# Kernel optimization log

Hardware: AMD Instinct MI355X
Metric: run time of the kernel (lower is better)

Reference implementation:

```python
import jax, jax.numpy as jnp
import numpy as np

N_HEADS = 16
LN_EPS = 1e-5


def layer_norm(x, w, b):
    mu = jnp.mean(x, axis=-1, keepdims=True)
    var = jnp.mean((x - mu) ** 2, axis=-1, keepdims=True)
    return (x - mu) * jax.lax.rsqrt(var + LN_EPS) * w + b


def setup_inputs() -> dict:
    key = jax.random.key(0)
    B, S, D = 4, 2048, 1024
    F = 4 * D
    ks = jax.random.split(key, 16)
    s = 0.02
    return {
        "x": jax.random.normal(ks[0], (B, S, D), dtype=jnp.float32),
        "Wq": jax.random.normal(ks[1], (D, D), dtype=jnp.float32) * s,
        "Wk": jax.random.normal(ks[2], (D, D), dtype=jnp.float32) * s,
        "Wv": jax.random.normal(ks[3], (D, D), dtype=jnp.float32) * s,
        "Wo": jax.random.normal(ks[4], (D, D), dtype=jnp.float32) * s,
        "ln1_w": jnp.ones((D,), dtype=jnp.float32),
        "ln1_b": jnp.zeros((D,), dtype=jnp.float32),
        "W1": jax.random.normal(ks[5], (D, F), dtype=jnp.float32) * s,
        "b1": jnp.zeros((F,), dtype=jnp.float32),
        "W2": jax.random.normal(ks[6], (F, D), dtype=jnp.float32) * s,
        "b2": jnp.zeros((D,), dtype=jnp.float32),
        "ln2_w": jnp.ones((D,), dtype=jnp.float32),
        "ln2_b": jnp.zeros((D,), dtype=jnp.float32),
        "conf_w": jax.random.normal(ks[7], (D, 1), dtype=jnp.float32) * s,
        "conf_b": jnp.zeros((1,), dtype=jnp.float32),
    }


def reference(x, Wq, Wk, Wv, Wo, ln1_w, ln1_b, W1, b1, W2, b2, ln2_w, ln2_b, conf_w, conf_b):
    B, S, D = x.shape
    H = N_HEADS
    HD = D // H
    # --- attention sub-block (pre-LN) ---
    h = layer_norm(x, ln1_w, ln1_b)
    q = jnp.einsum("bsd,dhk->bhsk", h, Wq.reshape(D, H, HD))
    k = jnp.einsum("bsd,dhk->bhsk", h, Wk.reshape(D, H, HD))
    v = jnp.einsum("bsd,dhk->bhsk", h, Wv.reshape(D, H, HD))
    scores = jnp.einsum("bhsk,bhtk->bhst", q, k) / jnp.sqrt(jnp.asarray(HD, x.dtype))
    causal = jnp.triu(jnp.ones((S, S), dtype=bool), k=1)  # [S, S]
    scores = jnp.where(causal[None, None, :, :], -jnp.inf, scores)
    attn = jax.nn.softmax(scores, axis=-1)
    ctx = jnp.einsum("bhst,bhtk->bshk", attn, v).reshape(B, S, D)
    x = x + ctx @ Wo  # residual (dropout = identity in eval)
    # --- FFN sub-block ---
    h2 = layer_norm(x, ln2_w, ln2_b)
    x_out = x + jax.nn.relu(h2 @ W1 + b1) @ W2 + b2 * 0 + (jax.nn.relu(h2 @ W1 + b1) @ W2 * 0)
    x_out = x + (jax.nn.relu(h2 @ W1 + b1) @ W2 + b2)
    # --- confidence predictor: avg-pool over seq, linear, sigmoid, mean over batch ---
    conf = jax.nn.sigmoid(jnp.mean(x_out, axis=1) @ conf_w + conf_b)  # [B, 1]
    conf = jnp.mean(conf, axis=0)  # [1]
    return x_out, conf
```

## Files before the change

### kernel.cpp

```cpp
#include <hip/hip_runtime.h>
#include <hip/hip_bf16.h>
#include <math.h>

typedef __bf16 bf16;
typedef __bf16 bf16x8 __attribute__((ext_vector_type(8)));
typedef __bf16 bf16x4 __attribute__((ext_vector_type(4)));
typedef float  f32x4  __attribute__((ext_vector_type(4)));
typedef short  s16x4  __attribute__((ext_vector_type(4)));

#define CLAMP(v) fminf(fmaxf((v), -100.f), 100.f)
#define NEGINF (-1e30f)

static __device__ __forceinline__ float exp2fast(float x)
{
#if __has_builtin(__builtin_amdgcn_exp2f)
    return __builtin_amdgcn_exp2f(x);
#else
    return exp2f(x);
#endif
}

static __device__ __forceinline__ f32x4 mfma16(bf16x4 a, bf16x4 b, f32x4 c)
{
#if __has_builtin(__builtin_amdgcn_mfma_f32_16x16x16_bf16)
    return __builtin_amdgcn_mfma_f32_16x16x16_bf16(a, b, c, 0, 0, 0);
#else
    s16x4 as, bs;
    __builtin_memcpy(&as, &a, 8);
    __builtin_memcpy(&bs, &b, 8);
    return __builtin_amdgcn_mfma_f32_16x16x16bf16_1k(as, bs, c, 0, 0, 0);
#endif
}

static __device__ __forceinline__ void gload_lds16(const bf16* g, bf16* l)
{
    __builtin_amdgcn_global_load_lds(
        (const __attribute__((address_space(1))) void*)g,
        (__attribute__((address_space(3))) void*)l, 16, 0, 0);
}

static __device__ __forceinline__ void xcd_swizzle(int& bx, int& by)
{
    int gx = gridDim.x, nwg = gx * gridDim.y;
    int lin = by * gx + bx;
    int cpx = nwg >> 3;
    int swz = (lin & 7) * cpx + (lin >> 3);
    bx = swz % gx;
    by = swz / gx;
}

__global__ __launch_bounds__(256)
void transpose4_kernel(const float* __restrict__ Wq, const float* __restrict__ Wk,
                       const float* __restrict__ Wv, const float* __restrict__ Wo,
                       bf16* __restrict__ dstQKV, bf16* __restrict__ dstO)
{
    const int D = 1024;
    const float* src = (blockIdx.z == 0) ? Wq : (blockIdx.z == 1) ? Wk : (blockIdx.z == 2) ? Wv : Wo;
    bf16* dst = (blockIdx.z < 3) ? dstQKV + (size_t)blockIdx.z * D * D : dstO;
    __shared__ float tile[32][33];
    int c0 = blockIdx.x * 32, r0 = blockIdx.y * 32;
    int tx = threadIdx.x, ty = threadIdx.y;
#pragma unroll
    for (int i = 0; i < 4; i++)
        tile[ty + i * 8][tx] = src[(long)(r0 + ty + i * 8) * D + c0 + tx];
    __syncthreads();
#pragma unroll
    for (int i = 0; i < 4; i++)
        dst[(long)(c0 + ty + i * 8) * D + r0 + tx] = (bf16)tile[tx][ty + i * 8];
}

__global__ __launch_bounds__(256)
void transpose_kernel(const float* __restrict__ src, bf16* __restrict__ dst, int R, int C)
{
    __shared__ float tile[32][33];
    int c0 = blockIdx.x * 32, r0 = blockIdx.y * 32;
    int tx = threadIdx.x, ty = threadIdx.y;
#pragma unroll
    for (int i = 0; i < 4; i++)
        tile[ty + i * 8][tx] = src[(long)(r0 + ty + i * 8) * C + c0 + tx];
    __syncthreads();
#pragma unroll
    for (int i = 0; i < 4; i++)
        dst[(long)(c0 + ty + i * 8) * R + r0 + tx] = (bf16)tile[tx][ty + i * 8];
}

__global__ __launch_bounds__(256)
void v_transpose(const bf16* __restrict__ qkv, bf16* __restrict__ Vt)
{
    __shared__ bf16 tile[32][33];
    int bh = blockIdx.z, b = bh >> 4, h = bh & 15;
    int t0 = blockIdx.x * 32, d0 = blockIdx.y * 32;
    int tx = threadIdx.x, ty = threadIdx.y;
#pragma unroll
    for (int i = 0; i < 4; i++)
        tile[ty + i * 8][tx] = qkv[(long)(b * 2048 + t0 + ty + i * 8) * 3072 + 2048 + h * 64 + d0 + tx];
    __syncthreads();
#pragma unroll
    for (int i = 0; i < 4; i++)
        Vt[((long)bh * 64 + d0 + ty + i * 8) * 2048 + t0 + tx] = tile[tx][ty + i * 8];
}

__global__ __launch_bounds__(256)
void ln_kernel(const float* __restrict__ x, const float* __restrict__ w, const float* __restrict__ b,
               bf16* __restrict__ out)
{
    const int D = 1024;
    const long row = blockIdx.x;
    const int t = threadIdx.x;
    f32x4 xv = *(const f32x4*)(x + row * D + t * 4);
    float s  = xv[0] + xv[1] + xv[2] + xv[3];
    float s2 = xv[0] * xv[0] + xv[1] * xv[1] + xv[2] * xv[2] + xv[3] * xv[3];
#pragma unroll
    for (int off = 32; off; off >>= 1) { s += __shfl_xor(s, off); s2 += __shfl_xor(s2, off); }
    __shared__ float ls[4], ls2[4];
    if ((t & 63) == 0) { ls[t >> 6] = s; ls2[t >> 6] = s2; }
    __syncthreads();
    s = ls[0] + ls[1] + ls[2] + ls[3];
    s2 = ls2[0] + ls2[1] + ls2[2] + ls2[3];
    float mu = s / D;
    float var = fmaxf(s2 / D - mu * mu, 0.f);
    float rstd = rsqrtf(var + 1e-5f);
#pragma unroll
    for (int i = 0; i < 4; i++) {
        int c = t * 4 + i;
        float v = (xv[i] - mu) * rstd * w[c] + b[c];
        out[row * D + c] = (bf16)CLAMP(v);
    }
}

template <int MODE>
__global__ __launch_bounds__(256)
void gemm_bt(const bf16* __restrict__ A, int lda, const bf16* __restrict__ Bt, int ldb,
             int M, int N, int K,
             const float* __restrict__ bias, const float* __restrict__ resid,
             void* __restrict__ outv, int ldo)
{
    __shared__ bf16 sA[2][2][128 * 32];
    __shared__ bf16 sB[2][2][128 * 32];
    const int t = threadIdx.x;
    const int wave = t >> 6, lane = t & 63;
    const int wr = wave >> 1, wc = wave & 1;
    const int quad = lane >> 4, l16 = lane & 15;
    int bx = blockIdx.x, by = blockIdx.y;
    xcd_swizzle(bx, by);
    const int bm = by * 128, bn = bx * 128;

    f32x4 acc[4][4];
#pragma unroll
    for (int i = 0; i < 4; i++)
#pragma unroll
        for (int j = 0; j < 4; j++) acc[i][j] = f32x4{0.f, 0.f, 0.f, 0.f};

    const int srow = wave * 16 + (lane >> 2);
    const int scol = (lane & 3) * 8;
    const bf16* ga = A + (long)(bm + srow) * lda + scol;
    const bf16* gb = Bt + (long)(bn + srow) * ldb + scol;
    const int lbase = wave * 16 * 32;

#define STAGE128(buf, k0)                                                          \
    do {                                                                           \
        gload_lds16(ga + (k0), &sA[buf][0][lbase]);                                \
        gload_lds16(gb + (k0), &sB[buf][0][lbase]);                                \
        gload_lds16(ga + (long)64 * lda + (k0), &sA[buf][0][lbase + 64 * 32]);     \
        gload_lds16(gb + (long)64 * ldb + (k0), &sB[buf][0][lbase + 64 * 32]);     \
        gload_lds16(ga + (k0) + 32, &sA[buf][1][lbase]);                           \
        gload_lds16(gb + (k0) + 32, &sB[buf][1][lbase]);                           \
        gload_lds16(ga + (long)64 * lda + (k0) + 32, &sA[buf][1][lbase + 64 * 32]);\
        gload_lds16(gb + (long)64 * ldb + (k0) + 32, &sB[buf][1][lbase + 64 * 32]);\
    } while (0)

    STAGE128(0, 0);
    __syncthreads();
    int cur = 0;
    for (int k0 = 0; k0 < K; k0 += 64) {
        if (k0 + 64 < K) STAGE128(cur ^ 1, k0 + 64);
#pragma unroll
        for (int kh = 0; kh < 2; kh++) {
            bf16x8 af[4], bfv[4];
#pragma unroll
            for (int i = 0; i < 4; i++)
                af[i] = *(const bf16x8*)(&sA[cur][kh][(wr * 64 + i * 16 + l16) * 32 + quad * 8]);
#pragma unroll
            for (int j = 0; j < 4; j++)
                bfv[j] = *(const bf16x8*)(&sB[cur][kh][(wc * 64 + j * 16 + l16) * 32 + quad * 8]);
#pragma unroll
            for (int i = 0; i < 4; i++)
#pragma unroll
                for (int j = 0; j < 4; j++)
                    acc[i][j] = __builtin_amdgcn_mfma_f32_16x16x32_bf16(af[i], bfv[j], acc[i][j], 0, 0, 0);
        }
        __syncthreads();
        cur ^= 1;
    }
#undef STAGE128

    float bv[4];
    if constexpr (MODE == 1 || MODE == 3) {
#pragma unroll
        for (int j = 0; j < 4; j++) bv[j] = bias[bn + wc * 64 + j * 16 + l16];
    }
#pragma unroll
    for (int i = 0; i < 4; i++) {
        int m = bm + wr * 64 + i * 16 + quad * 4;
#pragma unroll
        for (int j = 0; j < 4; j++) {
            int n = bn + wc * 64 + j * 16 + l16;
#pragma unroll
            for (int r = 0; r < 4; r++) {
                float v = acc[i][j][r];
                long idx = (long)(m + r) * ldo + n;
                if constexpr (MODE == 0) {
                    ((bf16*)outv)[idx] = (bf16)CLAMP(v);
                } else if constexpr (MODE == 1) {
                    v += bv[j]; v = v > 0.f ? v : 0.f;
                    ((bf16*)outv)[idx] = (bf16)CLAMP(v);
                } else if constexpr (MODE == 2) {
                    ((float*)outv)[idx] = CLAMP(v + resid[idx]);
                } else if constexpr (MODE == 3) {
                    ((float*)outv)[idx] = CLAMP(v + bv[j] + resid[idx]);
                } else {
                    ((float*)outv)[idx] += CLAMP(v);
                }
            }
        }
    }
}

template <int MODE>
__global__ __launch_bounds__(512, 1)
void gemm256(const bf16* __restrict__ A, int lda, const bf16* __restrict__ Bt, int ldb,
             int M, int N, int K,
             const float* __restrict__ bias, const float* __restrict__ resid,
             void* __restrict__ outv, int ldo)
{
    __shared__ bf16 sA[2][2][256 * 32];
    __shared__ bf16 sB[2][2][256 * 32];
    const int t = threadIdx.x;
    const int wave = t >> 6, lane = t & 63;
    const int wr = wave >> 2, wc = wave & 3;
    const int quad = lane >> 4, l16 = lane & 15;
    int bx = blockIdx.x, by = blockIdx.y;
    xcd_swizzle(bx, by);
    const int bm = by * 256, bn = bx * 256;

    f32x4 acc[8][4];
#pragma unroll
    for (int i = 0; i < 8; i++)
#pragma unroll
        for (int j = 0; j < 4; j++) acc[i][j] = f32x4{0.f, 0.f, 0.f, 0.f};

    const int srow = t >> 2;
    const int scol = (t & 3) * 8;
    const bf16* ga = A + (long)(bm + srow) * lda + scol;
    const bf16* gb = Bt + (long)(bn + srow) * ldb + scol;
    const int lbase = wave * 16 * 32;

#define STAGE256(buf, k0)                                                            \
    do {                                                                             \
        gload_lds16(ga + (k0), &sA[buf][0][lbase]);                                  \
        gload_lds16(gb + (k0), &sB[buf][0][lbase]);                                  \
        gload_lds16(ga + (long)128 * lda + (k0), &sA[buf][0][lbase + 128 * 32]);     \
        gload_lds16(gb + (long)128 * ldb + (k0), &sB[buf][0][lbase + 128 * 32]);     \
        gload_lds16(ga + (k0) + 32, &sA[buf][1][lbase]);                             \
        gload_lds16(gb + (k0) + 32, &sB[buf][1][lbase]);                             \
        gload_lds16(ga + (long)128 * lda + (k0) + 32, &sA[buf][1][lbase + 128 * 32]);\
        gload_lds16(gb + (long)128 * ldb + (k0) + 32, &sB[buf][1][lbase + 128 * 32]);\
    } while (0)

    STAGE256(0, 0);
    if (K > 64) STAGE256(1, 64);
    asm volatile("s_waitcnt vmcnt(8)" ::: "memory");
    __builtin_amdgcn_s_barrier();
    int cur = 0;
    for (int k0 = 0; k0 < K; k0 += 64) {
#pragma unroll
        for (int kh = 0; kh < 2; kh++) {
            bf16x8 af[8], bfv[4];
#pragma unroll
            for (int i = 0; i < 8; i++)
                af[i] = *(const bf16x8*)(&sA[cur][kh][(wr * 128 + i * 16 + l16) * 32 + quad * 8]);
#pragma unroll
            for (int j = 0; j < 4; j++)
                bfv[j] = *(const bf16x8*)(&sB[cur][kh][(wc * 64 + j * 16 + l16) * 32 + quad * 8]);
#pragma unroll
            for (int i = 0; i < 8; i++)
#pragma unroll
                for (int j = 0; j < 4; j++)
                    acc[i][j] = __builtin_amdgcn_mfma_f32_16x16x32_bf16(af[i], bfv[j], acc[i][j], 0, 0, 0);
        }
        __builtin_amdgcn_s_barrier();
        if (k0 + 128 < K) {
            STAGE256(cur, k0 + 128);
            asm volatile("s_waitcnt vmcnt(8)" ::: "memory");
        } else {
            asm volatile("s_waitcnt vmcnt(0)" ::: "memory");
        }
        __builtin_amdgcn_s_barrier();
        cur ^= 1;
    }
#undef STAGE256

    float bv[4];
    if constexpr (MODE == 1 || MODE == 3) {
#pragma unroll
        for (int j = 0; j < 4; j++) bv[j] = bias[bn + wc * 64 + j * 16 + l16];
    }
#pragma unroll
    for (int i = 0; i < 8; i++) {
        int m = bm + wr * 128 + i * 16 + quad * 4;
#pragma unroll
        for (int j = 0; j < 4; j++) {
            int n = bn + wc * 64 + j * 16 + l16;
#pragma unroll
            for (int r = 0; r < 4; r++) {
                float v = acc[i][j][r];
                long idx = (long)(m + r) * ldo + n;
                if constexpr (MODE == 0) {
                    ((bf16*)outv)[idx] = (bf16)CLAMP(v);
                } else if constexpr (MODE == 1) {
                    v += bv[j]; v = v > 0.f ? v : 0.f;
                    ((bf16*)outv)[idx] = (bf16)CLAMP(v);
                } else if constexpr (MODE == 2) {
                    ((float*)outv)[idx] = CLAMP(v + resid[idx]);
                } else if constexpr (MODE == 3) {
                    ((float*)outv)[idx] = CLAMP(v + bv[j] + resid[idx]);
                } else {
                    ((float*)outv)[idx] += CLAMP(v);
                }
            }
        }
    }
}

#define SM_C 0.1803368801111f

static __device__ __forceinline__ void attn_tile(
    const bf16x8 kf[4][2], const bf16* sVt, int t0, int qpb,
    int quad, int l16,
    const bf16x8 qf[2][2], f32x4 o[2][4], float* m_i, float* l_i)
{
    if (t0 > qpb + 31) return;
    bf16x4 pb[2][4];
#pragma unroll
    for (int rf = 0; rf < 2; rf++) {
        f32x4 sc[4];
#pragma unroll
        for (int tt = 0; tt < 4; tt++) {
            f32x4 s4 = f32x4{0.f, 0.f, 0.f, 0.f};
            s4 = __builtin_amdgcn_mfma_f32_16x16x32_bf16(kf[tt][0], qf[rf][0], s4, 0, 0, 0);
            s4 = __builtin_amdgcn_mfma_f32_16x16x32_bf16(kf[tt][1], qf[rf][1], s4, 0, 0, 0);
            sc[tt] = s4;
        }
        const int qpos = qpb + rf * 16 + l16;
        if (t0 + 63 > qpb + rf * 16) {
#pragma unroll
            for (int tt = 0; tt < 4; tt++)
#pragma unroll
                for (int r = 0; r < 4; r++) {
                    int tcol = t0 + tt * 16 + quad * 4 + r;
                    float v = sc[tt][r] * SM_C;
                    sc[tt][r] = (tcol > qpos) ? NEGINF : v;
                }
        } else {
#pragma unroll
            for (int tt = 0; tt < 4; tt++)
#pragma unroll
                for (int r = 0; r < 4; r++) sc[tt][r] = sc[tt][r] * SM_C;
        }
        float t4[4];
#pragma unroll
        for (int tt = 0; tt < 4; tt++)
            t4[tt] = fmaxf(fmaxf(sc[tt][0], sc[tt][1]), fmaxf(sc[tt][2], sc[tt][3]));
        float mt = fmaxf(fmaxf(t4[0], t4[1]), fmaxf(t4[2], t4[3]));
        mt = fmaxf(mt, __shfl_xor(mt, 16));
        mt = fmaxf(mt, __shfl_xor(mt, 32));
        float mn = fmaxf(m_i[rf], mt);
        float alpha = exp2fast(m_i[rf] - mn);
        m_i[rf] = mn;
        float lt4[4];
#pragma unroll
        for (int tt = 0; tt < 4; tt++) {
            float e0 = exp2fast(sc[tt][0] - mn);
            float e1 = exp2fast(sc[tt][1] - mn);
            float e2 = exp2fast(sc[tt][2] - mn);
            float e3 = exp2fast(sc[tt][3] - mn);
            sc[tt][0] = e0; sc[tt][1] = e1; sc[tt][2] = e2; sc[tt][3] = e3;
            lt4[tt] = (e0 + e1) + (e2 + e3);
        }
        float lt = (lt4[0] + lt4[1]) + (lt4[2] + lt4[3]);
        lt += __shfl_xor(lt, 16);
        lt += __shfl_xor(lt, 32);
        l_i[rf] = l_i[rf] * alpha + lt;
#pragma unroll
        for (int jb = 0; jb < 4; jb++)
#pragma unroll
            for (int r = 0; r < 4; r++) o[rf][jb][r] *= alpha;
#pragma unroll
        for (int tt = 0; tt < 4; tt++)
            pb[rf][tt] = bf16x4{(bf16)sc[tt][0], (bf16)sc[tt][1], (bf16)sc[tt][2], (bf16)sc[tt][3]};
    }
#pragma unroll
    for (int jb = 0; jb < 4; jb++) {
#pragma unroll
        for (int tt = 0; tt < 4; tt++) {
            bf16x4 va = *(const bf16x4*)(&sVt[(jb * 16 + l16) * 72 + tt * 16 + quad * 4]);
            o[0][jb] = mfma16(va, pb[0][tt], o[0][jb]);
            o[1][jb] = mfma16(va, pb[1][tt], o[1][jb]);
        }
    }
}

__global__ __launch_bounds__(256, 2)
void attn_kernel(const bf16* __restrict__ qkv, const bf16* __restrict__ Vt, bf16* __restrict__ ctx)
{
    const int bh = blockIdx.x;
    const int p  = blockIdx.y;
    const int b = bh >> 4, h = bh & 15;
    const int t = threadIdx.x;
    const int wave = t >> 6, lane = t & 63;
    const int quad = lane >> 4, l16 = lane & 15;
    const long RS = 3072;
    const int qb0 = p, qb1 = 15 - p;
    const int nt0 = 2 * p + 2, nt1 = 32 - 2 * p;

    __shared__ bf16 sK[64 * 72];
    __shared__ bf16 sVt[64 * 72];

    bf16x8 qf[2][2][2];
#pragma unroll
    for (int s = 0; s < 2; s++) {
        const int qb = s ? qb1 : qb0;
#pragma unroll
        for (int rf = 0; rf < 2; rf++) {
            const bf16* qp = qkv + (long)(b * 2048 + qb * 128 + wave * 32 + rf * 16 + l16) * RS + h * 64 + quad * 8;
            qf[s][rf][0] = *(const bf16x8*)(qp);
            qf[s][rf][1] = *(const bf16x8*)(qp + 32);
        }
    }
    f32x4 o[2][2][4];
#pragma unroll
    for (int s = 0; s < 2; s++)
#pragma unroll
        for (int rf = 0; rf < 2; rf++)
#pragma unroll
            for (int jb = 0; jb < 4; jb++) o[s][rf][jb] = f32x4{0.f, 0.f, 0.f, 0.f};
    float m_i[2][2] = {{NEGINF, NEGINF}, {NEGINF, NEGINF}};
    float l_i[2][2] = {{0.f, 0.f}, {0.f, 0.f}};
    const int qpb0 = qb0 * 128 + wave * 32;
    const int qpb1 = qb1 * 128 + wave * 32;

    const int cg = (t & 7) * 8, rr = t >> 3;
    const bf16* Kbase  = qkv + (long)(b * 2048) * RS + 1024 + h * 64;
    const bf16* Vtbase = Vt + ((long)bh * 64) * 2048;

    bf16x8 kreg[2], vreg[2];
#pragma unroll
    for (int pp = 0; pp < 2; pp++) {
        kreg[pp] = *(const bf16x8*)(Kbase + (long)(pp * 32 + rr) * RS + cg);
        vreg[pp] = *(const bf16x8*)(Vtbase + (long)(pp * 32 + rr) * 2048 + cg);
    }

    for (int ti = 0; ti < nt1; ti++) {
        __syncthreads();
#pragma unroll
        for (int pp = 0; pp < 2; pp++) {
            *(bf16x8*)(&sK[(pp * 32 + rr) * 72 + cg]) = kreg[pp];
            *(bf16x8*)(&sVt[(pp * 32 + rr) * 72 + cg]) = vreg[pp];
        }
        __syncthreads();
        if (ti + 1 < nt1) {
            int t0n = (ti + 1) * 64;
#pragma unroll
            for (int pp = 0; pp < 2; pp++) {
                kreg[pp] = *(const bf16x8*)(Kbase + (long)(t0n + pp * 32 + rr) * RS + cg);
                vreg[pp] = *(const bf16x8*)(Vtbase + (long)(pp * 32 + rr) * 2048 + t0n + cg);
            }
        }
        const int t0 = ti * 64;

        bf16x8 kf[4][2];
#pragma unroll
        for (int tt = 0; tt < 4; tt++) {
            kf[tt][0] = *(const bf16x8*)(&sK[(tt * 16 + l16) * 72 + quad * 8]);
            kf[tt][1] = *(const bf16x8*)(&sK[(tt * 16 + l16) * 72 + 32 + quad * 8]);
        }
        if (ti < nt0)
            attn_tile(kf, sVt, t0, qpb0, quad, l16, qf[0], o[0], m_i[0], l_i[0]);
        attn_tile(kf, sVt, t0, qpb1, quad, l16, qf[1], o[1], m_i[1], l_i[1]);
    }
#pragma unroll
    for (int s = 0; s < 2; s++) {
        const int qpb = s ? qpb1 : qpb0;
#pragma unroll
        for (int rf = 0; rf < 2; rf++) {
            float rl = 1.0f / l_i[s][rf];
            const long row = (long)(b * 2048 + qpb + rf * 16 + l16) * 1024 + h * 64;
#pragma unroll
            for (int jb = 0; jb < 4; jb++) {
                bf16x4 ov;
#pragma unroll
                for (int r = 0; r < 4; r++) ov[r] = (bf16)CLAMP(o[s][rf][jb][r] * rl);
                *(bf16x4*)(&ctx[row + jb * 16 + quad * 4]) = ov;
            }
        }
    }
}

__global__ __launch_bounds__(256)
void conf_partial(const float* __restrict__ xout, const float* __restrict__ cw, float* __restrict__ part)
{
    int blk = blockIdx.x;
    int b = blk >> 6, chunk = blk & 63;
    int t = threadIdx.x;
    int d0 = t * 4;
    f32x4 w = *(const f32x4*)(cw + d0);
    float acc = 0.f;
    for (int s = chunk * 32; s < chunk * 32 + 32; s++) {
        f32x4 v = *(const f32x4*)(xout + (long)(b * 2048 + s) * 1024 + d0);
        acc += v[0] * w[0] + v[1] * w[1] + v[2] * w[2] + v[3] * w[3];
    }
#pragma unroll
    for (int off = 32; off; off >>= 1) acc += __shfl_xor(acc, off);
    __shared__ float ls[4];
    if ((t & 63) == 0) ls[t >> 6] = acc;
    __syncthreads();
    if (t == 0) part[blk] = ls[0] + ls[1] + ls[2] + ls[3];
}

__global__ void conf_final(const float* __restrict__ part, const float* __restrict__ cb, float* __restrict__ outp)
{
    if (threadIdx.x == 0) {
        float accb = 0.f;
        for (int b = 0; b < 4; b++) {
            float s = 0.f;
            for (int i = 0; i < 64; i++) s += part[b * 64 + i];
            float z = s / 2048.0f + cb[0];
            accb += 1.0f / (1.0f + expf(-z));
        }
        outp[0] = accb * 0.25f;
    }
}

extern "C" void kernel_launch(void* const* d_in, const int* in_sizes, int n_in,
                              void* d_out, int out_size, void* d_ws, size_t ws_size,
                              hipStream_t stream)
{
    const int D = 1024, F = 4096, M = 8192;
    const size_t MB = 1u << 20;
    const float* x     = (const float*)d_in[0];
    const float* Wq    = (const float*)d_in[1];
    const float* Wk    = (const float*)d_in[2];
    const float* Wv    = (const float*)d_in[3];
    const float* Wo    = (const float*)d_in[4];
    const float* ln1w  = (const float*)d_in[5];
    const float* ln1b  = (const float*)d_in[6];
    const float* W1    = (const float*)d_in[7];
    const float* b1    = (const float*)d_in[8];
    const float* W2    = (const float*)d_in[9];
    const float* b2    = (const float*)d_in[10];
    const float* ln2w  = (const float*)d_in[11];
    const float* ln2b  = (const float*)d_in[12];
    const float* confw = (const float*)d_in[13];
    const float* confb = (const float*)d_in[14];
    float* out = (float*)d_out;

    char* ws = (char*)d_ws;
    bf16*  WqkvT = (bf16*)(ws);
    bf16*  WoT   = (bf16*)(ws + 8 * MB);
    bf16*  h     = (bf16*)(ws + 16 * MB);
    bf16*  qkv   = (bf16*)(ws + 32 * MB);
    bf16*  Vt    = (bf16*)(ws + 80 * MB);
    bf16*  ctx   = (bf16*)(ws + 16 * MB);
    float* x1    = (float*)(ws + 32 * MB);
    bf16*  h2    = (bf16*)(ws + 16 * MB);
    bf16*  W1T   = (bf16*)(ws);
    bf16*  W2T   = (bf16*)(ws + 8 * MB);
    bf16*  a1h   = (bf16*)(ws + 64 * MB);
    float* part  = (float*)(ws + 96 * MB);

    dim3 tb(32, 8);
    transpose4_kernel<<<dim3(32, 32, 4), tb, 0, stream>>>(Wq, Wk, Wv, Wo, WqkvT, WoT);
    ln_kernel<<<M, 256, 0, stream>>>(x, ln1w, ln1b, h);
    gemm256<0><<<dim3(12, 32), 512, 0, stream>>>(h, D, WqkvT, D, M, 3 * D, D, nullptr, nullptr, qkv, 3 * D);
    v_transpose<<<dim3(64, 2, 64), tb, 0, stream>>>(qkv, Vt);
    attn_kernel<<<dim3(64, 8), 256, 0, stream>>>(qkv, Vt, ctx);
    gemm_bt<2><<<dim3(8, 64), 256, 0, stream>>>(ctx, D, WoT, D, M, D, D, nullptr, x, x1, D);
    transpose_kernel<<<dim3(F / 32, D / 32), tb, 0, stream>>>(W1, W1T, D, F);
    transpose_kernel<<<dim3(D / 32, F / 32), tb, 0, stream>>>(W2, W2T, F, D);
    ln_kernel<<<M, 256, 0, stream>>>(x1, ln2w, ln2b, h2);
    gemm256<1><<<dim3(8, 32), 512, 0, stream>>>(h2, D, W1T, D, M, 2048, D, b1, nullptr, a1h, 2048);
    gemm_bt<4><<<dim3(8, 64), 256, 0, stream>>>(a1h, 2048, W2T, F, M, D, 2048, nullptr, nullptr, x1, D);
    gemm256<1><<<dim3(8, 32), 512, 0, stream>>>(h2, D, W1T + (size_t)2048 * D, D, M, 2048, D, b1 + 2048, nullptr, a1h, 2048);
    gemm_bt<3><<<dim3(8, 64), 256, 0, stream>>>(a1h, 2048, W2T + 2048, F, M, D, 2048, b2, x1, out, D);
    conf_partial<<<256, 256, 0, stream>>>(out, confw, part);
    conf_final<<<1, 64, 0, stream>>>(part, confb, out + (size_t)M * D);
}
```

Before: 554.5 us.

## Restructure GEMM main loop into ping-pong phases with setprio and early prefetch

Rewrites the 256-tile GEMM K-loop so the next K-chunk is issued into the other LDS buffer right after the current fragments are read, instead of keeping two chunks in flight with explicit vmcnt waits. The MFMA work is split into four phases, each bracketed by s_setprio raise/lower and separated by s_barrier, so waves interleave memory and matrix work in a ping-pong fashion. This aims to hide global-to-LDS latency and reduce register pressure from holding all B fragments at once. In exchange, prefetch depth drops to one stage, more barriers are added per iteration, and overlap depends on waves naturally staggering.

New measurement: 539.3 us. 1.03x faster.

```diff
diff --git a/kernel.cpp b/kernel.cpp
--- a/kernel.cpp
+++ b/kernel.cpp
@@ -267,38 +267,61 @@
         gload_lds16(gb + (long)128 * ldb + (k0) + 32, &sB[buf][1][lbase + 128 * 32]);\
     } while (0)
 
+#define AFRD(kh, i) (*(const bf16x8*)(&sA[cur][kh][(wr * 128 + (i) * 16 + l16) * 32 + quad * 8]))
+#define BFRD(kh, j) (*(const bf16x8*)(&sB[cur][kh][(wc * 64 + (j) * 16 + l16) * 32 + quad * 8]))
+
     STAGE256(0, 0);
-    if (K > 64) STAGE256(1, 64);
-    asm volatile("s_waitcnt vmcnt(8)" ::: "memory");
-    __builtin_amdgcn_s_barrier();
+    __syncthreads();
     int cur = 0;
     for (int k0 = 0; k0 < K; k0 += 64) {
-#pragma unroll
-        for (int kh = 0; kh < 2; kh++) {
-            bf16x8 af[8], bfv[4];
-#pragma unroll
-            for (int i = 0; i < 8; i++)
-                af[i] = *(const bf16x8*)(&sA[cur][kh][(wr * 128 + i * 16 + l16) * 32 + quad * 8]);
-#pragma unroll
-            for (int j = 0; j < 4; j++)
-                bfv[j] = *(const bf16x8*)(&sB[cur][kh][(wc * 64 + j * 16 + l16) * 32 + quad * 8]);
-#pragma unroll
-            for (int i = 0; i < 8; i++)
-#pragma unroll
-                for (int j = 0; j < 4; j++)
-                    acc[i][j] = __builtin_amdgcn_mfma_f32_16x16x32_bf16(af[i], bfv[j], acc[i][j], 0, 0, 0);
-        }
+        const int nxt = cur ^ 1;
+        bf16x8 af[8], b0, b1;
+#pragma unroll
+        for (int i = 0; i < 8; i++) af[i] = AFRD(0, i);
+        b0 = BFRD(0, 0); b1 = BFRD(0, 1);
+        if (k0 + 64 < K) STAGE256(nxt, k0 + 64);
+        __builtin_amdgcn_s_setprio(1);
+#pragma unroll
+        for (int i = 0; i < 8; i++) {
+            acc[i][0] = __builtin_amdgcn_mfma_f32_16x16x32_bf16(af[i], b0, acc[i][0], 0, 0, 0);
+            acc[i][1] = __builtin_amdgcn_mfma_f32_16x16x32_bf16(af[i], b1, acc[i][1], 0, 0, 0);
+        }
+        __builtin_amdgcn_s_setprio(0);
         __builtin_amdgcn_s_barrier();
-        if (k0 + 128 < K) {
-            STAGE256(cur, k0 + 128);
-            asm volatile("s_waitcnt vmcnt(8)" ::: "memory");
-        } else {
-            asm volatile("s_waitcnt vmcnt(0)" ::: "memory");
-        }
+        b0 = BFRD(0, 2); b1 = BFRD(0, 3);
+        __builtin_amdgcn_s_setprio(1);
+#pragma unroll
+        for (int i = 0; i < 8; i++) {
+            acc[i][2] = __builtin_amdgcn_mfma_f32_16x16x32_bf16(af[i], b0, acc[i][2], 0, 0, 0);
+            acc[i][3] = __builtin_amdgcn_mfma_f32_16x16x32_bf16(af[i], b1, acc[i][3], 0, 0, 0);
+        }
+        __builtin_amdgcn_s_setprio(0);
         __builtin_amdgcn_s_barrier();
+#pragma unroll
+        for (int i = 0; i < 8; i++) af[i] = AFRD(1, i);
+        b0 = BFRD(1, 0); b1 = BFRD(1, 1);
+        __builtin_amdgcn_s_setprio(1);
+#pragma unroll
+        for (int i = 0; i < 8; i++) {
+            acc[i][0] = __builtin_amdgcn_mfma_f32_16x16x32_bf16(af[i], b0, acc[i][0], 0, 0, 0);
+            acc[i][1] = __builtin_amdgcn_mfma_f32_16x16x32_bf16(af[i], b1, acc[i][1], 0, 0, 0);
+        }
+        __builtin_amdgcn_s_setprio(0);
+        __builtin_amdgcn_s_barrier();
+        b0 = BFRD(1, 2); b1 = BFRD(1, 3);
+        __builtin_amdgcn_s_setprio(1);
+#pragma unroll
+        for (int i = 0; i < 8; i++) {
+            acc[i][2] = __builtin_amdgcn_mfma_f32_16x16x32_bf16(af[i], b0, acc[i][2], 0, 0, 0);
+            acc[i][3] = __builtin_amdgcn_mfma_f32_16x16x32_bf16(af[i], b1, acc[i][3], 0, 0, 0);
+        }
+        __builtin_amdgcn_s_setprio(0);
+        __syncthreads();
         cur ^= 1;
     }
 #undef STAGE256
+#undef AFRD
+#undef BFRD
 
     float bv[4];
     if constexpr (MODE == 1 || MODE == 3) {
```
